# Performance work log

Measured on AMD Instinct MI355X. Metric: run time of the kernel, lower is better.

The kernel has to match this reference:

```python
import jax, jax.numpy as jnp
import numpy as np

ATTN_SIZE = 64
ENC_SIZE = 512
HIDDEN_SIZE = 512
L, B = 2048, 64


def setup_inputs() -> dict:
    key = jax.random.key(0)
    k1, k2, k3, k4, k5, k6 = jax.random.split(key, 6)
    enc_outputs = jax.random.normal(k1, (L, B, ENC_SIZE), dtype=jnp.float32)
    lens = jax.random.randint(k2, (B,), 1, L + 1, dtype=jnp.int32)
    hidden_states = jax.random.normal(k3, (B, HIDDEN_SIZE), dtype=jnp.float32)
    # Xavier-normal params as in reset_params()
    W_enc = jax.random.normal(k4, (ENC_SIZE, ATTN_SIZE), dtype=jnp.float32) * np.sqrt(2.0 / (ENC_SIZE + ATTN_SIZE))
    W_hidden = jax.random.normal(k5, (HIDDEN_SIZE, ATTN_SIZE), dtype=jnp.float32) * np.sqrt(2.0 / (HIDDEN_SIZE + ATTN_SIZE))
    b_attn = jnp.zeros((ATTN_SIZE,), dtype=jnp.float32)
    v = jax.random.normal(k6, (ATTN_SIZE,), dtype=jnp.float32)
    return {"enc_outputs": enc_outputs, "lens": lens, "hidden_states": hidden_states,
            "W_enc": W_enc, "b_attn": b_attn, "W_hidden": W_hidden, "v": v}


def reference(enc_outputs, lens, hidden_states, W_enc, b_attn, W_hidden, v):
    l = enc_outputs.shape[0]
    # parts: (l, b, attn_size) — projection of encoder outputs
    parts = jnp.einsum('lbd,da->lba', enc_outputs, W_enc) + b_attn
    # additive (Bahdanau) score: tanh(parts + h @ W_hidden) . v -> (l, b)
    hid = hidden_states @ W_hidden  # (b, attn_size)
    scores = jnp.sum(jnp.tanh(parts + hid[None, :, :]) * v, axis=2)
    # faithful mask: 1.0 at valid positions, -inf at padding (original adds 1, a
    # constant shift that softmax cancels, but we reproduce the exact math)
    valid = jnp.arange(l, dtype=lens.dtype)[:, None] < lens[None, :]  # (l, b)
    mask = jnp.where(valid, jnp.float32(1.0), -jnp.inf)
    w = jax.nn.softmax(scores + mask, axis=0)  # softmax over sequence dim
    # weighted sum over sequence: (b, d)
    return jnp.einsum('lb,lbd->bd', w, enc_outputs)
```

## Files before the change

kernel.cpp:

```cpp
#include <hip/hip_runtime.h>
#include <hip/hip_bf16.h>
#include <math.h>

#define L_DIM 2048
#define B_DIM 64
#define D_DIM 512
#define A_DIM 64

#define SUB_L 16
#define CHUNK_L 64
#define N_SUB (CHUNK_L / SUB_L)
#define N_CHUNK (L_DIM / CHUNK_L)
#define EPAD 520

typedef __attribute__((ext_vector_type(8))) short bf16x8;
typedef __attribute__((ext_vector_type(4))) float f32x4;

__device__ __forceinline__ void split_bf16(float x, short& hi, short& lo) {
    __hip_bfloat16 h = __float2bfloat16(x);
    float hf = __bfloat162float(h);
    __hip_bfloat16 l = __float2bfloat16(x - hf);
    hi = *reinterpret_cast<short*>(&h);
    lo = *reinterpret_cast<short*>(&l);
}

__device__ __forceinline__ void split4(const float4& x, short4& h, short4& l) {
    split_bf16(x.x, h.x, l.x);
    split_bf16(x.y, h.y, l.y);
    split_bf16(x.z, h.z, l.z);
    split_bf16(x.w, h.w, l.w);
}

__device__ __forceinline__ float bf_hi_lo(short h, short l) {
    unsigned uh = ((unsigned)(unsigned short)h) << 16;
    unsigned ul = ((unsigned)(unsigned short)l) << 16;
    return __uint_as_float(uh) + __uint_as_float(ul);
}

__device__ __forceinline__ void lds_barrier() {
    asm volatile("s_waitcnt lgkmcnt(0)" ::: "memory");
    __builtin_amdgcn_s_barrier();
}

__global__ void hb_kernel(const float* __restrict__ hidden,
                          const float* __restrict__ Wh,
                          const float* __restrict__ battn,
                          float* __restrict__ hb) {
    const int b = blockIdx.x;
    const int a = threadIdx.x;
    const float* hrow = hidden + b * D_DIM;
    float acc = battn[a];
#pragma unroll 8
    for (int d = 0; d < D_DIM; ++d) acc += hrow[d] * Wh[d * A_DIM + a];
    hb[b * A_DIM + a] = acc;
}

__global__ __launch_bounds__(256) void wt_kernel(const float* __restrict__ We,
                                                 short* __restrict__ wt_hi,
                                                 short* __restrict__ wt_lo) {
    const int idx = blockIdx.x * 256 + threadIdx.x;
    const int a = idx & 63;
    const int d = idx >> 6;
    float x = We[d * A_DIM + a];
    short h, l;
    split_bf16(x, h, l);
    wt_hi[a * D_DIM + d] = h;
    wt_lo[a * D_DIM + d] = l;
}

__global__ __launch_bounds__(256, 2) void fused_kernel(
    const float* __restrict__ enc, const short* __restrict__ wt_hi,
    const short* __restrict__ wt_lo, const float* __restrict__ hb,
    const float* __restrict__ v, const int* __restrict__ lens,
    float* __restrict__ Om, float* __restrict__ mz) {
    const int c = blockIdx.x;
    const int b = blockIdx.y;
    const int tid = threadIdx.x;
    const int wave = tid >> 6;
    const int lane = tid & 63;
    const int quad = lane >> 4;
    const int l15 = lane & 15;
    const int po = tid & 127;
    const int par = tid >> 7;

    __shared__ short Ehi[2][SUB_L][EPAD];
    __shared__ short Elo[2][SUB_L][EPAD];
    __shared__ float sred[SUB_L][4];
    __shared__ float wl[SUB_L];
    __shared__ float msc[2];
    __shared__ float ored[D_DIM];

    const int len_b = lens[b];
    const int a_col = wave * 16 + l15;
    const float hb0 = hb[b * A_DIM + a_col];
    const float v0 = v[a_col];

    const short* bh = wt_hi + (size_t)a_col * D_DIM + quad * 8;
    const short* bl = wt_lo + (size_t)a_col * D_DIM + quad * 8;
    bf16x8 Bh[16], Bl[16];
#pragma unroll
    for (int s = 0; s < 16; ++s) {
        Bh[s] = *(const bf16x8*)(bh + s * 32);
        Bl[s] = *(const bf16x8*)(bl + s * 32);
    }

    float4 Oacc = {0.f, 0.f, 0.f, 0.f};
    float mA = -INFINITY, ZA = 0.f;

    const float* encb = enc + (size_t)c * CHUNK_L * B_DIM * D_DIM +
                        (size_t)b * D_DIM + po * 4;
    const size_t ROWSTRIDE = (size_t)B_DIM * D_DIM;

    float4 buf[8];
#pragma unroll
    for (int j = 0; j < 8; ++j)
        buf[j] = *(const float4*)(encb + (size_t)(2 * j + par) * ROWSTRIDE);

#pragma unroll 2
    for (int sub = 0; sub < N_SUB; ++sub) {
        const int cb = sub & 1;

#pragma unroll
        for (int j = 0; j < 8; ++j) {
            const int li = 2 * j + par;
            short4 h4, l4;
            split4(buf[j], h4, l4);
            *(short4*)&Ehi[cb][li][po * 4] = h4;
            *(short4*)&Elo[cb][li][po * 4] = l4;
        }
        lds_barrier();

        if (sub + 1 < N_SUB) {
            const float* p = encb + (size_t)(sub + 1) * SUB_L * ROWSTRIDE;
#pragma unroll
            for (int j = 0; j < 8; ++j)
                buf[j] = *(const float4*)(p + (size_t)(2 * j + par) * ROWSTRIDE);
        }

        f32x4 a0 = {0.f, 0.f, 0.f, 0.f};
        f32x4 a1 = {0.f, 0.f, 0.f, 0.f};
        f32x4 a2 = {0.f, 0.f, 0.f, 0.f};
#pragma unroll
        for (int s = 0; s < 16; ++s) {
            const int k = s * 32;
            const bf16x8 Ah = *(const bf16x8*)&Ehi[cb][l15][k + quad * 8];
            const bf16x8 Al = *(const bf16x8*)&Elo[cb][l15][k + quad * 8];
            a0 = __builtin_amdgcn_mfma_f32_16x16x32_bf16(Ah, Bh[s], a0, 0, 0, 0);
            a1 = __builtin_amdgcn_mfma_f32_16x16x32_bf16(Ah, Bl[s], a1, 0, 0, 0);
            a2 = __builtin_amdgcn_mfma_f32_16x16x32_bf16(Al, Bh[s], a2, 0, 0, 0);
        }

#pragma unroll
        for (int r = 0; r < 4; ++r) {
            float t = tanhf(a0[r] + a1[r] + a2[r] + hb0) * v0;
            t += __shfl_xor(t, 1);
            t += __shfl_xor(t, 2);
            t += __shfl_xor(t, 4);
            t += __shfl_xor(t, 8);
            if (l15 == 0) sred[quad * 4 + r][wave] = t;
        }
        lds_barrier();

        if (tid < SUB_L) {
            const int lg = c * CHUNK_L + sub * SUB_L + tid;
            float s = sred[tid][0] + sred[tid][1] + sred[tid][2] + sred[tid][3];
            s = (lg < len_b) ? (s + 1.0f) : -INFINITY;
            float m = s;
            m = fmaxf(m, __shfl_xor(m, 1));
            m = fmaxf(m, __shfl_xor(m, 2));
            m = fmaxf(m, __shfl_xor(m, 4));
            m = fmaxf(m, __shfl_xor(m, 8));
            const float w = (m == -INFINITY) ? 0.f : expf(s - m);
            wl[tid] = w;
            float z = w;
            z += __shfl_xor(z, 1);
            z += __shfl_xor(z, 2);
            z += __shfl_xor(z, 4);
            z += __shfl_xor(z, 8);
            if (tid == 0) { msc[0] = m; msc[1] = z; }
        }
        lds_barrier();

        const float m_sub = msc[0], Z_sub = msc[1];
        const float mN = fmaxf(mA, m_sub);
        const float cA = (mA == -INFINITY) ? 0.f : expf(mA - mN);
        const float cS = (m_sub == -INFINITY) ? 0.f : expf(m_sub - mN);
        Oacc.x *= cA; Oacc.y *= cA; Oacc.z *= cA; Oacc.w *= cA;
#pragma unroll
        for (int j = 0; j < 8; ++j) {
            const int li = 2 * j + par;
            const float w = cS * wl[li];
            const short4 h4 = *(const short4*)&Ehi[cb][li][po * 4];
            const short4 l4 = *(const short4*)&Elo[cb][li][po * 4];
            Oacc.x += w * bf_hi_lo(h4.x, l4.x);
            Oacc.y += w * bf_hi_lo(h4.y, l4.y);
            Oacc.z += w * bf_hi_lo(h4.z, l4.z);
            Oacc.w += w * bf_hi_lo(h4.w, l4.w);
        }
        ZA = cA * ZA + cS * Z_sub;
        mA = mN;
    }

    if (par == 0) *(float4*)&ored[po * 4] = Oacc;
    __syncthreads();
    if (par == 1) {
        const float4 o0 = *(const float4*)&ored[po * 4];
        float4 r;
        r.x = o0.x + Oacc.x;
        r.y = o0.y + Oacc.y;
        r.z = o0.z + Oacc.z;
        r.w = o0.w + Oacc.w;
        *(float4*)(Om + ((size_t)b * N_CHUNK + c) * D_DIM + po * 4) = r;
    }
    if (tid == 0) {
        mz[((size_t)b * N_CHUNK + c) * 2 + 0] = mA;
        mz[((size_t)b * N_CHUNK + c) * 2 + 1] = ZA;
    }
}

__global__ __launch_bounds__(256) void combine_kernel(
    const float* __restrict__ Om, const float* __restrict__ mz,
    float* __restrict__ out) {
    const int b = blockIdx.x;
    const int tid = threadIdx.x;
    __shared__ float coef[N_CHUNK];
    __shared__ float sinv;

    if (tid < 32) {
        const float m = mz[((size_t)b * N_CHUNK + tid) * 2 + 0];
        const float Z = mz[((size_t)b * N_CHUNK + tid) * 2 + 1];
        float mm = m;
        mm = fmaxf(mm, __shfl_xor(mm, 1));
        mm = fmaxf(mm, __shfl_xor(mm, 2));
        mm = fmaxf(mm, __shfl_xor(mm, 4));
        mm = fmaxf(mm, __shfl_xor(mm, 8));
        mm = fmaxf(mm, __shfl_xor(mm, 16));
        const float cc = (m == -INFINITY) ? 0.f : expf(m - mm);
        coef[tid] = cc;
        float s = cc * Z;
        s += __shfl_xor(s, 1);
        s += __shfl_xor(s, 2);
        s += __shfl_xor(s, 4);
        s += __shfl_xor(s, 8);
        s += __shfl_xor(s, 16);
        if (tid == 0) sinv = 1.0f / s;
    }
    __syncthreads();

    const float* base = Om + (size_t)b * N_CHUNK * D_DIM + tid * 2;
    float ox = 0.f, oy = 0.f;
#pragma unroll 8
    for (int cc = 0; cc < N_CHUNK; ++cc) {
        const float2 x = *(const float2*)(base + cc * D_DIM);
        ox += coef[cc] * x.x;
        oy += coef[cc] * x.y;
    }
    const float s = sinv;
    *(float2*)(out + (size_t)b * D_DIM + tid * 2) = make_float2(ox * s, oy * s);
}

extern "C" void kernel_launch(void* const* d_in, const int* in_sizes, int n_in,
                              void* d_out, int out_size, void* d_ws, size_t ws_size,
                              hipStream_t stream) {
    const float* enc    = (const float*)d_in[0];
    const int*   lens   = (const int*)d_in[1];
    const float* hidden = (const float*)d_in[2];
    const float* We     = (const float*)d_in[3];
    const float* battn  = (const float*)d_in[4];
    const float* Wh     = (const float*)d_in[5];
    const float* v      = (const float*)d_in[6];
    float* out = (float*)d_out;

    char* w8 = (char*)d_ws;
    float* hb    = (float*)(w8 + 0);
    short* wt_hi = (short*)(w8 + 16 * 1024);
    short* wt_lo = (short*)(w8 + 80 * 1024);
    float* mz    = (float*)(w8 + 144 * 1024);
    float* Om    = (float*)(w8 + 160 * 1024);

    hb_kernel<<<B_DIM, A_DIM, 0, stream>>>(hidden, Wh, battn, hb);
    wt_kernel<<<(D_DIM * A_DIM) / 256, 256, 0, stream>>>(We, wt_hi, wt_lo);
    fused_kernel<<<dim3(N_CHUNK, B_DIM), 256, 0, stream>>>(
        enc, wt_hi, wt_lo, hb, v, lens, Om, mz);
    combine_kernel<<<B_DIM, 256, 0, stream>>>(Om, mz, out);
}
```

Before: 436.3 us.

## Merge setup kernels, truncate-split via perm, fast tanh/exp, drop softmax barrier

Merges the hidden projection and weight transpose/split into one setup launch, and splits the hidden dot product across four waves. In the main kernel, the bf16 hi/lo split now uses truncation plus byte permutes instead of round-to-nearest conversions. tanh and exp are replaced with fast intrinsics. The per-subtile softmax is computed redundantly in every wave, with weights broadcast by shuffles, which removes one LDS barrier and the shared staging arrays. These cut instruction count and a sync in the hot loop, at the cost of slightly lower accuracy in tanh/exp and in the truncated hi/lo split.

```diff
diff --git a/kernel.cpp b/kernel.cpp
--- a/kernel.cpp
+++ b/kernel.cpp
@@ -24,11 +24,14 @@
     lo = *reinterpret_cast<short*>(&l);
 }
 
-__device__ __forceinline__ void split4(const float4& x, short4& h, short4& l) {
-    split_bf16(x.x, h.x, l.x);
-    split_bf16(x.y, h.y, l.y);
-    split_bf16(x.z, h.z, l.z);
-    split_bf16(x.w, h.w, l.w);
+__device__ __forceinline__ void split_pair(float x, float y,
+                                           unsigned& hi2, unsigned& lo2) {
+    unsigned ux = __float_as_uint(x), uy = __float_as_uint(y);
+    hi2 = __builtin_amdgcn_perm(uy, ux, 0x07060302u);
+    float rx = x - __uint_as_float(ux & 0xFFFF0000u);
+    float ry = y - __uint_as_float(uy & 0xFFFF0000u);
+    lo2 = __builtin_amdgcn_perm(__float_as_uint(ry), __float_as_uint(rx),
+                                0x07060302u);
 }
 
 __device__ __forceinline__ float bf_hi_lo(short h, short l) {
@@ -37,35 +40,49 @@
     return __uint_as_float(uh) + __uint_as_float(ul);
 }
 
+__device__ __forceinline__ float fast_tanh(float x) {
+    float e = __expf(2.0f * x);
+    return 1.0f - 2.0f / (e + 1.0f);
+}
+
 __device__ __forceinline__ void lds_barrier() {
     asm volatile("s_waitcnt lgkmcnt(0)" ::: "memory");
     __builtin_amdgcn_s_barrier();
 }
 
-__global__ void hb_kernel(const float* __restrict__ hidden,
-                          const float* __restrict__ Wh,
-                          const float* __restrict__ battn,
-                          float* __restrict__ hb) {
-    const int b = blockIdx.x;
-    const int a = threadIdx.x;
-    const float* hrow = hidden + b * D_DIM;
-    float acc = battn[a];
+__global__ __launch_bounds__(256) void setup_kernel(
+    const float* __restrict__ hidden, const float* __restrict__ Wh,
+    const float* __restrict__ battn, const float* __restrict__ We,
+    float* __restrict__ hb, short* __restrict__ wt_hi,
+    short* __restrict__ wt_lo) {
+    __shared__ float part[4][A_DIM];
+    if (blockIdx.x < 64) {
+        const int b = blockIdx.x;
+        const int a = threadIdx.x & 63;
+        const int sl = threadIdx.x >> 6;
+        const float* hrow = hidden + b * D_DIM + sl * 128;
+        const float* wcol = Wh + (size_t)sl * 128 * A_DIM + a;
+        float acc = 0.f;
 #pragma unroll 8
-    for (int d = 0; d < D_DIM; ++d) acc += hrow[d] * Wh[d * A_DIM + a];
-    hb[b * A_DIM + a] = acc;
-}
-
-__global__ __launch_bounds__(256) void wt_kernel(const float* __restrict__ We,
-                                                 short* __restrict__ wt_hi,
-                                                 short* __restrict__ wt_lo) {
-    const int idx = blockIdx.x * 256 + threadIdx.x;
-    const int a = idx & 63;
-    const int d = idx >> 6;
-    float x = We[d * A_DIM + a];
-    short h, l;
-    split_bf16(x, h, l);
-    wt_hi[a * D_DIM + d] = h;
-    wt_lo[a * D_DIM + d] = l;
+        for (int d = 0; d < 128; ++d) acc += hrow[d] * wcol[(size_t)d * A_DIM];
+        part[sl][a] = acc;
+        __syncthreads();
+        if (sl == 0)
+            hb[b * A_DIM + a] =
+                battn[a] + part[0][a] + part[1][a] + part[2][a] + part[3][a];
+    } else {
+        const int base = (blockIdx.x - 64) * 1024 + threadIdx.x * 4;
+#pragma unroll
+        for (int t = 0; t < 4; ++t) {
+            const int i = base + t;
+            const int a = i & 63;
+            const int d = i >> 6;
+            short h, l;
+            split_bf16(We[i], h, l);
+            wt_hi[a * D_DIM + d] = h;
+            wt_lo[a * D_DIM + d] = l;
+        }
+    }
 }
 
 __global__ __launch_bounds__(256, 2) void fused_kernel(
@@ -86,8 +103,6 @@
     __shared__ short Ehi[2][SUB_L][EPAD];
     __shared__ short Elo[2][SUB_L][EPAD];
     __shared__ float sred[SUB_L][4];
-    __shared__ float wl[SUB_L];
-    __shared__ float msc[2];
     __shared__ float ored[D_DIM];
 
     const int len_b = lens[b];
@@ -123,10 +138,11 @@
 #pragma unroll
         for (int j = 0; j < 8; ++j) {
             const int li = 2 * j + par;
-            short4 h4, l4;
-            split4(buf[j], h4, l4);
-            *(short4*)&Ehi[cb][li][po * 4] = h4;
-            *(short4*)&Elo[cb][li][po * 4] = l4;
+            uint2 h2, l2;
+            split_pair(buf[j].x, buf[j].y, h2.x, l2.x);
+            split_pair(buf[j].z, buf[j].w, h2.y, l2.y);
+            *(uint2*)&Ehi[cb][li][po * 4] = h2;
+            *(uint2*)&Elo[cb][li][po * 4] = l2;
         }
         lds_barrier();
 
@@ -152,7 +168,7 @@
 
 #pragma unroll
         for (int r = 0; r < 4; ++r) {
-            float t = tanhf(a0[r] + a1[r] + a2[r] + hb0) * v0;
+            float t = fast_tanh(a0[r] + a1[r] + a2[r] + hb0) * v0;
             t += __shfl_xor(t, 1);
             t += __shfl_xor(t, 2);
             t += __shfl_xor(t, 4);
@@ -161,43 +177,37 @@
         }
         lds_barrier();
 
-        if (tid < SUB_L) {
-            const int lg = c * CHUNK_L + sub * SUB_L + tid;
-            float s = sred[tid][0] + sred[tid][1] + sred[tid][2] + sred[tid][3];
-            s = (lg < len_b) ? (s + 1.0f) : -INFINITY;
-            float m = s;
-            m = fmaxf(m, __shfl_xor(m, 1));
-            m = fmaxf(m, __shfl_xor(m, 2));
-            m = fmaxf(m, __shfl_xor(m, 4));
-            m = fmaxf(m, __shfl_xor(m, 8));
-            const float w = (m == -INFINITY) ? 0.f : expf(s - m);
-            wl[tid] = w;
-            float z = w;
-            z += __shfl_xor(z, 1);
-            z += __shfl_xor(z, 2);
-            z += __shfl_xor(z, 4);
-            z += __shfl_xor(z, 8);
-            if (tid == 0) { msc[0] = m; msc[1] = z; }
-        }
-        lds_barrier();
-
-        const float m_sub = msc[0], Z_sub = msc[1];
-        const float mN = fmaxf(mA, m_sub);
-        const float cA = (mA == -INFINITY) ? 0.f : expf(mA - mN);
-        const float cS = (m_sub == -INFINITY) ? 0.f : expf(m_sub - mN);
+        float s = sred[l15][0] + sred[l15][1] + sred[l15][2] + sred[l15][3];
+        const int lg = c * CHUNK_L + sub * SUB_L + l15;
+        s = (lg < len_b) ? (s + 1.0f) : -INFINITY;
+        float m = s;
+        m = fmaxf(m, __shfl_xor(m, 1));
+        m = fmaxf(m, __shfl_xor(m, 2));
+        m = fmaxf(m, __shfl_xor(m, 4));
+        m = fmaxf(m, __shfl_xor(m, 8));
+        const float w = (m == -INFINITY) ? 0.f : __expf(s - m);
+        float z = w;
+        z += __shfl_xor(z, 1);
+        z += __shfl_xor(z, 2);
+        z += __shfl_xor(z, 4);
+        z += __shfl_xor(z, 8);
+
+        const float mN = fmaxf(mA, m);
+        const float cA = (mA == -INFINITY) ? 0.f : __expf(mA - mN);
+        const float cS = (m == -INFINITY) ? 0.f : __expf(m - mN);
         Oacc.x *= cA; Oacc.y *= cA; Oacc.z *= cA; Oacc.w *= cA;
 #pragma unroll
         for (int j = 0; j < 8; ++j) {
             const int li = 2 * j + par;
-            const float w = cS * wl[li];
+            const float wgt = cS * __shfl(w, li);
             const short4 h4 = *(const short4*)&Ehi[cb][li][po * 4];
             const short4 l4 = *(const short4*)&Elo[cb][li][po * 4];
-            Oacc.x += w * bf_hi_lo(h4.x, l4.x);
-            Oacc.y += w * bf_hi_lo(h4.y, l4.y);
-            Oacc.z += w * bf_hi_lo(h4.z, l4.z);
-            Oacc.w += w * bf_hi_lo(h4.w, l4.w);
-        }
-        ZA = cA * ZA + cS * Z_sub;
+            Oacc.x += wgt * bf_hi_lo(h4.x, l4.x);
+            Oacc.y += wgt * bf_hi_lo(h4.y, l4.y);
+            Oacc.z += wgt * bf_hi_lo(h4.z, l4.z);
+            Oacc.w += wgt * bf_hi_lo(h4.w, l4.w);
+        }
+        ZA = cA * ZA + cS * z;
         mA = mN;
     }
 
@@ -235,7 +245,7 @@
         mm = fmaxf(mm, __shfl_xor(mm, 4));
         mm = fmaxf(mm, __shfl_xor(mm, 8));
         mm = fmaxf(mm, __shfl_xor(mm, 16));
-        const float cc = (m == -INFINITY) ? 0.f : expf(m - mm);
+        const float cc = (m == -INFINITY) ? 0.f : __expf(m - mm);
         coef[tid] = cc;
         float s = cc * Z;
         s += __shfl_xor(s, 1);
@@ -278,8 +288,7 @@
     float* mz    = (float*)(w8 + 144 * 1024);
     float* Om    = (float*)(w8 + 160 * 1024);
 
-    hb_kernel<<<B_DIM, A_DIM, 0, stream>>>(hidden, Wh, battn, hb);
-    wt_kernel<<<(D_DIM * A_DIM) / 256, 256, 0, stream>>>(We, wt_hi, wt_lo);
+    setup_kernel<<<96, 256, 0, stream>>>(hidden, Wh, battn, We, hb, wt_hi, wt_lo);
     fused_kernel<<<dim3(N_CHUNK, B_DIM), 256, 0, stream>>>(
         enc, wt_hi, wt_lo, hb, v, lens, Om, mz);
     combine_kernel<<<B_DIM, 256, 0, stream>>>(Om, mz, out);
```

Measured after the change: 419.1 us. 3.9% less time.
